# Kernel tuning notes

Measured on AMD Instinct MI355X. Metric: run time of the kernel, lower is better.

## Reference

```python
import jax, jax.numpy as jnp
import numpy as np
from functools import partial


def lstm(x, Wx, Wh, b, act):
    """Keras LSTM. x:[B,T,F]. Gate order i,f,c,o. Returns (all_h:[B,T,H], last_h:[B,H])."""
    B, T, _ = x.shape
    H = Wh.shape[0]
    xz = jnp.einsum('btf,fg->btg', x, Wx) + b  # precompute input projections
    def step(carry, xz_t):
        h, c = carry
        z = xz_t + h @ Wh
        i, f, g, o = jnp.split(z, 4, axis=-1)
        i = jax.nn.sigmoid(i); f = jax.nn.sigmoid(f)
        g = act(g); o = jax.nn.sigmoid(o)
        c = f * c + i * g
        h = o * act(c)
        return (h, c), h
    init = (jnp.zeros((B, H), x.dtype), jnp.zeros((B, H), x.dtype))
    (h_last, _), hs = jax.lax.scan(step, init, jnp.swapaxes(xz, 0, 1))
    return jnp.swapaxes(hs, 0, 1), h_last


def gru(x, Wx, Wh, b):
    """Keras GRU with reset_after=True. b:[2,3H]. Gate order z,r,h. Returns last h."""
    B, T, _ = x.shape
    H = Wh.shape[0]
    xz = jnp.einsum('btf,fg->btg', x, Wx) + b[0]
    def step(h, xz_t):
        rec = h @ Wh + b[1]
        xz_z, xz_r, xz_h = jnp.split(xz_t, 3, axis=-1)
        r_z, r_r, r_h = jnp.split(rec, 3, axis=-1)
        z = jax.nn.sigmoid(xz_z + r_z)
        r = jax.nn.sigmoid(xz_r + r_r)
        hh = jnp.tanh(xz_h + r * r_h)
        h = z * h + (1.0 - z) * hh
        return h, None
    h0 = jnp.zeros((B, H), x.dtype)
    h_last, _ = jax.lax.scan(step, h0, jnp.swapaxes(xz, 0, 1))
    return h_last


def setup_inputs() -> dict:
    key = jax.random.key(0)
    ks = jax.random.split(key, 32)
    s = 0.05  # small init so relu-LSTM stays numerically stable over 64 steps
    d = {}
    d['keypoint_data'] = jax.random.normal(ks[0], (256, 64, 1662), jnp.float32)
    d['img_data'] = jax.random.normal(ks[1], (256, 64, 2048), jnp.float32)
    # keypoint LSTM stack: 1662->64->128->64, gates=4H
    d['kW1x'] = s * jax.random.normal(ks[2], (1662, 256), jnp.float32)
    d['kW1h'] = s * jax.random.normal(ks[3], (64, 256), jnp.float32)
    d['kb1'] = jnp.zeros((256,), jnp.float32)
    d['kW2x'] = s * jax.random.normal(ks[4], (64, 512), jnp.float32)
    d['kW2h'] = s * jax.random.normal(ks[5], (128, 512), jnp.float32)
    d['kb2'] = jnp.zeros((512,), jnp.float32)
    d['kW3x'] = s * jax.random.normal(ks[6], (128, 256), jnp.float32)
    d['kW3h'] = s * jax.random.normal(ks[7], (64, 256), jnp.float32)
    d['kb3'] = jnp.zeros((256,), jnp.float32)
    # keypoint dense heads
    d['kD1w'] = s * jax.random.normal(ks[8], (64, 64), jnp.float32)
    d['kD1b'] = jnp.zeros((64,), jnp.float32)
    d['kD2w'] = s * jax.random.normal(ks[9], (64, 32), jnp.float32)
    d['kD2b'] = jnp.zeros((32,), jnp.float32)
    # img branch: LSTM 2048->64 (tanh), GRU 64->8 (reset_after bias [2,24])
    d['iWx'] = s * jax.random.normal(ks[10], (2048, 256), jnp.float32)
    d['iWh'] = s * jax.random.normal(ks[11], (64, 256), jnp.float32)
    d['ib'] = jnp.zeros((256,), jnp.float32)
    d['gWx'] = s * jax.random.normal(ks[12], (64, 24), jnp.float32)
    d['gWh'] = s * jax.random.normal(ks[13], (8, 24), jnp.float32)
    d['gb'] = jnp.zeros((2, 24), jnp.float32)
    d['iDw'] = s * jax.random.normal(ks[14], (8, 8), jnp.float32)
    d['iDb'] = jnp.zeros((8,), jnp.float32)
    # final dense on concat([img(8), key(32)]) -> num_classes
    d['fW'] = s * jax.random.normal(ks[15], (40, 10), jnp.float32)
    d['fb'] = jnp.zeros((10,), jnp.float32)
    return d


def reference(keypoint_data, img_data,
              kW1x, kW1h, kb1, kW2x, kW2h, kb2, kW3x, kW3h, kb3,
              kD1w, kD1b, kD2w, kD2b,
              iWx, iWh, ib, gWx, gWh, gb, iDw, iDb, fW, fb):
    relu = jax.nn.relu
    # keypoint branch: 3 relu-LSTMs
    h, _ = lstm(keypoint_data, kW1x, kW1h, kb1, relu)
    h, _ = lstm(h, kW2x, kW2h, kb2, relu)
    _, h = lstm(h, kW3x, kW3h, kb3, relu)  # return_sequences=False
    h = relu(h @ kD1w + kD1b)
    key_out = relu(h @ kD2w + kD2b)  # [B,32]
    # img branch: tanh LSTM -> GRU -> (dropout=identity at inference) -> dense
    hs, _ = lstm(img_data, iWx, iWh, ib, jnp.tanh)
    g = gru(hs, gWx, gWh, gb)  # [B,8]
    img_out = relu(g @ iDw + iDb)  # [B,8]
    combined = jnp.concatenate([img_out, key_out], axis=-1)  # [B,40]
    return jax.nn.softmax(combined @ fW + fb, axis=-1)
```

## Files before the change

### kernel.cpp

```cpp
#include <hip/hip_runtime.h>


typedef short bf16x8 __attribute__((ext_vector_type(8)));
typedef float f32x4 __attribute__((ext_vector_type(4)));

__device__ __forceinline__ unsigned f2bf(float x) {
    unsigned u = __float_as_uint(x);
    return (u + 0x7FFFu + ((u >> 16) & 1u)) >> 16;
}
__device__ __forceinline__ float bf2f(unsigned b) { return __uint_as_float(b << 16); }
__device__ __forceinline__ float sigmoidf_(float x) { return 1.f / (1.f + __expf(-x)); }
__device__ __forceinline__ float tanhf_(float x) {
    float e = __expf(2.f * x);
    return 1.f - 2.f / (e + 1.f);
}

template<int K, int N>
__device__ __forceinline__ void split_w(const float* __restrict__ W,
                                        unsigned short* __restrict__ hi,
                                        unsigned short* __restrict__ lo, int item) {
    int kt = item / N;
    int n  = item % N;
    unsigned uh[16], ul[16];
#pragma unroll
    for (int p = 0; p < 16; p++) {
        unsigned h2[2], l2[2];
#pragma unroll
        for (int e = 0; e < 2; e++) {
            int k = kt * 32 + p * 2 + e;
            float x = (k < K) ? W[(size_t)k * N + n] : 0.f;
            unsigned hb = f2bf(x);
            h2[e] = hb;
            l2[e] = f2bf(x - bf2f(hb));
        }
        uh[p] = h2[0] | (h2[1] << 16);
        ul[p] = l2[0] | (l2[1] << 16);
    }
    size_t off = (size_t)(kt * N + n) * 32;
    uint4* dh = (uint4*)(hi + off);
    uint4* dl = (uint4*)(lo + off);
#pragma unroll
    for (int c = 0; c < 4; c++) {
        uint4 v; v.x = uh[c*4]; v.y = uh[c*4+1]; v.z = uh[c*4+2]; v.w = uh[c*4+3];
        dh[c] = v;
        uint4 u; u.x = ul[c*4]; u.y = ul[c*4+1]; u.z = ul[c*4+2]; u.w = ul[c*4+3];
        dl[c] = u;
    }
}

__global__ __launch_bounds__(256) void split_all(
    const float* kW1x, const float* iWx, const float* kW2x, const float* kW3x,
    unsigned short* w1h, unsigned short* w1l, unsigned short* wih, unsigned short* wil,
    unsigned short* w2h, unsigned short* w2l, unsigned short* w3h, unsigned short* w3l) {
    int wid = blockIdx.x * 256 + threadIdx.x;
    if (wid < 13312)       split_w<1662, 256>(kW1x, w1h, w1l, wid);
    else if (wid < 29696)  split_w<2048, 256>(iWx,  wih, wil, wid - 13312);
    else if (wid < 30720)  split_w<64,   512>(kW2x, w2h, w2l, wid - 29696);
    else if (wid < 31744)  split_w<128,  256>(kW3x, w3h, w3l, wid - 30720);
}

__global__ __launch_bounds__(256, 2) void gemm_rd(
    const float* __restrict__ A, const unsigned short* __restrict__ Bhi,
    const unsigned short* __restrict__ Blo, const float* __restrict__ bias,
    float* __restrict__ out0, float* __restrict__ out1,
    int Kreal, int Kt, int Nfull) {
    const int m0  = blockIdx.x * 64;
    const int n0  = blockIdx.y * 256;
    const int ks  = blockIdx.z;
    const int nks = gridDim.z;
    const int ktChunk = (Kt + nks - 1) / nks;
    const int kt0 = ks * ktChunk;
    const int ktEnd = min(Kt, kt0 + ktChunk);
    const int tid = threadIdx.x;
    const int lane = tid & 63;
    const int wv   = tid >> 6;
    const int l15  = lane & 15;
    const int q    = lane >> 4;

    __shared__ unsigned short Ah[2][64 * 40], Al[2][64 * 40];

    f32x4 acc[4][4];
#pragma unroll
    for (int i = 0; i < 4; i++)
#pragma unroll
        for (int j = 0; j < 4; j++) acc[i][j] = (f32x4){0.f, 0.f, 0.f, 0.f};

    auto stage = [&](int kt, int buf) {
#pragma unroll
        for (int it = 0; it < 2; it++) {
            int item = tid + it * 256;
            int row = item >> 3, kg = item & 7;
            int gk = kt * 32 + kg * 4;
            const float* ap = A + (size_t)(m0 + row) * Kreal + gk;
            float x0, x1, x2, x3;
            if (gk + 4 <= Kreal) {
                float2 p0 = *(const float2*)ap;
                float2 p1 = *(const float2*)(ap + 2);
                x0 = p0.x; x1 = p0.y; x2 = p1.x; x3 = p1.y;
            } else {
                x0 = (gk + 0 < Kreal) ? ap[0] : 0.f;
                x1 = (gk + 1 < Kreal) ? ap[1] : 0.f;
                x2 = (gk + 2 < Kreal) ? ap[2] : 0.f;
                x3 = (gk + 3 < Kreal) ? ap[3] : 0.f;
            }
            unsigned h0 = f2bf(x0), h1 = f2bf(x1), h2 = f2bf(x2), h3 = f2bf(x3);
            unsigned l0 = f2bf(x0 - bf2f(h0)), l1 = f2bf(x1 - bf2f(h1));
            unsigned l2 = f2bf(x2 - bf2f(h2)), l3 = f2bf(x3 - bf2f(h3));
            uint2 vh; vh.x = h0 | (h1 << 16); vh.y = h2 | (h3 << 16);
            uint2 vl; vl.x = l0 | (l1 << 16); vl.y = l2 | (l3 << 16);
            *(uint2*)&Ah[buf][row * 40 + kg * 4] = vh;
            *(uint2*)&Al[buf][row * 40 + kg * 4] = vl;
        }
    };

    stage(kt0, 0);
    for (int kt = kt0; kt < ktEnd; kt++) {
        int b = (kt - kt0) & 1;
        bf16x8 bh[4], bl[4];
#pragma unroll
        for (int nt = 0; nt < 4; nt++) {
            size_t boff = ((size_t)kt * Nfull + n0 + wv * 64 + nt * 16 + l15) * 32 + q * 8;
            bh[nt] = *(const bf16x8*)(Bhi + boff);
            bl[nt] = *(const bf16x8*)(Blo + boff);
        }
        __syncthreads();
        if (kt + 1 < ktEnd) stage(kt + 1, b ^ 1);
#pragma unroll
        for (int mt = 0; mt < 4; mt++) {
            int o = (mt * 16 + l15) * 40 + q * 8;
            bf16x8 ah = *(const bf16x8*)&Ah[b][o];
            bf16x8 al = *(const bf16x8*)&Al[b][o];
#pragma unroll
            for (int nt = 0; nt < 4; nt++) {
                acc[mt][nt] = __builtin_amdgcn_mfma_f32_16x16x32_bf16(ah, bh[nt], acc[mt][nt], 0, 0, 0);
                acc[mt][nt] = __builtin_amdgcn_mfma_f32_16x16x32_bf16(ah, bl[nt], acc[mt][nt], 0, 0, 0);
                acc[mt][nt] = __builtin_amdgcn_mfma_f32_16x16x32_bf16(al, bh[nt], acc[mt][nt], 0, 0, 0);
            }
        }
    }
    float* op = (ks == 0) ? out0 : out1;
#pragma unroll
    for (int nt = 0; nt < 4; nt++) {
        int gcol = n0 + wv * 64 + nt * 16 + l15;
        float bv = (ks == 0) ? bias[gcol] : 0.f;
#pragma unroll
        for (int mt = 0; mt < 4; mt++)
#pragma unroll
            for (int r = 0; r < 4; r++) {
                int grow = m0 + mt * 16 + q * 4 + r;
                op[(size_t)grow * Nfull + gcol] = acc[mt][nt][r] + bv;
            }
    }
}

__global__ __launch_bounds__(256) void lstm_h64(
    int nA,
    const float* __restrict__ xA0, const float* __restrict__ xA1,
    const float* __restrict__ WhA, float* __restrict__ hA, int actA,
    const float* __restrict__ xB0, const float* __restrict__ xB1,
    const float* __restrict__ WhB, float* __restrict__ hB, int actB) {
    int bid = blockIdx.x;
    bool sec = bid >= nA;
    int b = sec ? bid - nA : bid;
    const float* x0 = sec ? xB0 : xA0;
    const float* x1 = sec ? xB1 : xA1;
    const float* Wh = sec ? WhB : WhA;
    float* hout     = sec ? hB  : hA;
    int act         = sec ? actB : actA;
    bool has1 = (x1 != nullptr);

    int g = threadIdx.x;
    float w[64];
#pragma unroll
    for (int k = 0; k < 64; k++) w[k] = Wh[k * 256 + g];

    __shared__ alignas(16) float hs[64];
    __shared__ float za[256];
    if (g < 64) hs[g] = 0.f;
    float c = 0.f;
    __syncthreads();

    const float* x0r = x0 + (size_t)b * 64 * 256;
    const float* x1r = has1 ? x1 + (size_t)b * 64 * 256 : x0r;
    float* hr = hout + (size_t)b * 64 * 64;
    bool isc = (g >= 128) && (g < 192);
    float cur = x0r[g] + (has1 ? x1r[g] : 0.f);
    for (int t = 0; t < 64; t++) {
        float nxt = 0.f;
        if (t < 63) {
            nxt = x0r[(t + 1) * 256 + g];
            if (has1) nxt += x1r[(t + 1) * 256 + g];
        }
        float z0 = cur, z1 = 0.f, z2 = 0.f, z3 = 0.f;
#pragma unroll
        for (int kk = 0; kk < 16; kk++) {
            float4 h4 = *(const float4*)&hs[kk * 4];
            float a0 = fmaf(h4.x, w[kk * 4 + 0], fmaf(h4.y, w[kk * 4 + 1], 0.f));
            float a1 = fmaf(h4.z, w[kk * 4 + 2], fmaf(h4.w, w[kk * 4 + 3], 0.f));
            if ((kk & 3) == 0) { z0 += a0; z1 += a1; }
            else if ((kk & 3) == 1) { z2 += a0; z3 += a1; }
            else if ((kk & 3) == 2) { z0 += a0; z1 += a1; }
            else { z2 += a0; z3 += a1; }
        }
        float z = (z0 + z1) + (z2 + z3);
        float a;
        if (isc) a = (act == 0) ? fmaxf(z, 0.f) : tanhf_(z);
        else     a = sigmoidf_(z);
        za[g] = a;
        __syncthreads();
        if (g < 64) {
            float iv = za[g], fv = za[64 + g], cd = za[128 + g], ov = za[192 + g];
            c = fmaf(fv, c, iv * cd);
            float ca = (act == 0) ? fmaxf(c, 0.f) : tanhf_(c);
            float h = ov * ca;
            hs[g] = h;
            hr[t * 64 + g] = h;
        }
        __syncthreads();
        cur = nxt;
    }
}

__global__ __launch_bounds__(512, 2) void lstm_h128(
    const float* __restrict__ xz, const float* __restrict__ Wh, float* __restrict__ hout) {
    int b = blockIdx.x;
    int g = threadIdx.x;
    float w[128];
#pragma unroll
    for (int k = 0; k < 128; k++) w[k] = Wh[k * 512 + g];

    __shared__ alignas(16) float hs[128];
    __shared__ float za[512];
    if (g < 128) hs[g] = 0.f;
    float c = 0.f;
    __syncthreads();

    const float* xzr = xz + (size_t)b * 64 * 512;
    float* hr = hout + (size_t)b * 64 * 128;
    bool isc = (g >= 256) && (g < 384);
    float cur = xzr[g];
    for (int t = 0; t < 64; t++) {
        float nxt = 0.f;
        if (t < 63) nxt = xzr[(t + 1) * 512 + g];
        float z0 = cur, z1 = 0.f, z2 = 0.f, z3 = 0.f;
#pragma unroll
        for (int kk = 0; kk < 32; kk++) {
            float4 h4 = *(const float4*)&hs[kk * 4];
            float a0 = fmaf(h4.x, w[kk * 4 + 0], fmaf(h4.y, w[kk * 4 + 1], 0.f));
            float a1 = fmaf(h4.z, w[kk * 4 + 2], fmaf(h4.w, w[kk * 4 + 3], 0.f));
            if ((kk & 1) == 0) { z0 += a0; z1 += a1; }
            else { z2 += a0; z3 += a1; }
        }
        float z = (z0 + z1) + (z2 + z3);
        float a = isc ? fmaxf(z, 0.f) : sigmoidf_(z);
        za[g] = a;
        __syncthreads();
        if (g < 128) {
            float iv = za[g], fv = za[128 + g], cd = za[256 + g], ov = za[384 + g];
            c = fmaf(fv, c, iv * cd);
            float h = ov * fmaxf(c, 0.f);
            hs[g] = h;
            hr[t * 128 + g] = h;
        }
        __syncthreads();
        cur = nxt;
    }
}

__global__ __launch_bounds__(64) void gru_kernel(
    const float* __restrict__ hsimg, const float* __restrict__ gWx,
    const float* __restrict__ gWh, const float* __restrict__ gb,
    float* __restrict__ glast) {
    int b = blockIdx.x;
    int qq = threadIdx.x;
    int col = (qq < 24) ? qq : 0;
    float wx[64], wh[8];
#pragma unroll
    for (int k = 0; k < 64; k++) wx[k] = gWx[k * 24 + col];
#pragma unroll
    for (int k = 0; k < 8; k++)  wh[k] = gWh[k * 24 + col];
    float b0 = gb[col], b1 = gb[24 + col];

    float hval = 0.f;
    const float* hb = hsimg + (size_t)b * 64 * 64;
    for (int t = 0; t < 64; t++) {
        float s0 = b0, s1 = 0.f, s2 = 0.f, s3 = 0.f;
#pragma unroll
        for (int k = 0; k < 64; k += 4) {
            s0 = fmaf(hb[t * 64 + k + 0], wx[k + 0], s0);
            s1 = fmaf(hb[t * 64 + k + 1], wx[k + 1], s1);
            s2 = fmaf(hb[t * 64 + k + 2], wx[k + 2], s2);
            s3 = fmaf(hb[t * 64 + k + 3], wx[k + 3], s3);
        }
        float sx = (s0 + s1) + (s2 + s3);
        float sr = b1;
#pragma unroll
        for (int k = 0; k < 8; k++) sr = fmaf(__shfl(hval, k), wh[k], sr);
        float xzz = __shfl(sx, qq),      rzz = __shfl(sr, qq);
        float xzr = __shfl(sx, 8 + qq),  rzr = __shfl(sr, 8 + qq);
        float xzh = __shfl(sx, 16 + qq), rzh = __shfl(sr, 16 + qq);
        float zz = sigmoidf_(xzz + rzz);
        float rv = sigmoidf_(xzr + rzr);
        float hc = tanhf_(xzh + rv * rzh);
        hval = zz * hval + (1.f - zz) * hc;
    }
    if (qq < 8) glast[b * 8 + qq] = hval;
}

__global__ __launch_bounds__(64) void final_head(
    const float* __restrict__ h3seq, const float* __restrict__ glast,
    const float* __restrict__ kD1w, const float* __restrict__ kD1b,
    const float* __restrict__ kD2w, const float* __restrict__ kD2b,
    const float* __restrict__ iDw,  const float* __restrict__ iDb,
    const float* __restrict__ fW,   const float* __restrict__ fb,
    float* __restrict__ outp) {
    int b = blockIdx.x * 64 + threadIdx.x;
    float h3[64];
#pragma unroll
    for (int k = 0; k < 64; k++) h3[k] = h3seq[((size_t)b * 64 + 63) * 64 + k];
    float d1[64];
#pragma unroll
    for (int j = 0; j < 64; j++) {
        float s = kD1b[j];
#pragma unroll
        for (int k = 0; k < 64; k++) s = fmaf(h3[k], kD1w[k * 64 + j], s);
        d1[j] = fmaxf(s, 0.f);
    }
    float d2[32];
#pragma unroll
    for (int j = 0; j < 32; j++) {
        float s = kD2b[j];
#pragma unroll
        for (int k = 0; k < 64; k++) s = fmaf(d1[k], kD2w[k * 32 + j], s);
        d2[j] = fmaxf(s, 0.f);
    }
    float gi[8];
#pragma unroll
    for (int k = 0; k < 8; k++) gi[k] = glast[b * 8 + k];
    float io[8];
#pragma unroll
    for (int j = 0; j < 8; j++) {
        float s = iDb[j];
#pragma unroll
        for (int k = 0; k < 8; k++) s = fmaf(gi[k], iDw[k * 8 + j], s);
        io[j] = fmaxf(s, 0.f);
    }
    float lg[10];
#pragma unroll
    for (int j = 0; j < 10; j++) {
        float s = fb[j];
#pragma unroll
        for (int k = 0; k < 8; k++)  s = fmaf(io[k], fW[k * 10 + j], s);
#pragma unroll
        for (int k = 0; k < 32; k++) s = fmaf(d2[k], fW[(8 + k) * 10 + j], s);
        lg[j] = s;
    }
    float mx = lg[0];
#pragma unroll
    for (int j = 1; j < 10; j++) mx = fmaxf(mx, lg[j]);
    float den = 0.f, ex[10];
#pragma unroll
    for (int j = 0; j < 10; j++) { ex[j] = __expf(lg[j] - mx); den += ex[j]; }
    float inv = 1.f / den;
#pragma unroll
    for (int j = 0; j < 10; j++) outp[b * 10 + j] = ex[j] * inv;
}

extern "C" void kernel_launch(void* const* d_in, const int* in_sizes, int n_in,
                              void* d_out, int out_size, void* d_ws, size_t ws_size,
                              hipStream_t stream) {
    const float* keypoint = (const float*)d_in[0];
    const float* img      = (const float*)d_in[1];
    const float* kW1x = (const float*)d_in[2];
    const float* kW1h = (const float*)d_in[3];
    const float* kb1  = (const float*)d_in[4];
    const float* kW2x = (const float*)d_in[5];
    const float* kW2h = (const float*)d_in[6];
    const float* kb2  = (const float*)d_in[7];
    const float* kW3x = (const float*)d_in[8];
    const float* kW3h = (const float*)d_in[9];
    const float* kb3  = (const float*)d_in[10];
    const float* kD1w = (const float*)d_in[11];
    const float* kD1b = (const float*)d_in[12];
    const float* kD2w = (const float*)d_in[13];
    const float* kD2b = (const float*)d_in[14];
    const float* iWx  = (const float*)d_in[15];
    const float* iWh  = (const float*)d_in[16];
    const float* ib   = (const float*)d_in[17];
    const float* gWx  = (const float*)d_in[18];
    const float* gWh  = (const float*)d_in[19];
    const float* gb   = (const float*)d_in[20];
    const float* iDw  = (const float*)d_in[21];
    const float* iDb  = (const float*)d_in[22];
    const float* fW   = (const float*)d_in[23];
    const float* fb   = (const float*)d_in[24];
    float* outp = (float*)d_out;

    char* ws = (char*)d_ws;
    const size_t MB16 = (size_t)16384 * 256 * 4;
    float* r1a = (float*)(ws);
    float* r1b = (float*)(ws + MB16);
    float* r2a = (float*)(ws + 2 * MB16);
    float* r2b = (float*)(ws + 3 * MB16);
    size_t off = 4 * MB16;
    float* h1seq = (float*)(ws + off); off += (size_t)16384 * 64 * 4;
    float* h2seq = (float*)(ws + off); off += (size_t)16384 * 128 * 4;
    float* hsimg = (float*)(ws + off); off += (size_t)16384 * 64 * 4;
    float* glast = (float*)(ws + off); off += (size_t)256 * 8 * 4;
    unsigned short* w1h = (unsigned short*)(ws + off); off += (size_t)52 * 256 * 32 * 2;
    unsigned short* w1l = (unsigned short*)(ws + off); off += (size_t)52 * 256 * 32 * 2;
    unsigned short* wih = (unsigned short*)(ws + off); off += (size_t)64 * 256 * 32 * 2;
    unsigned short* wil = (unsigned short*)(ws + off); off += (size_t)64 * 256 * 32 * 2;
    unsigned short* w2h = (unsigned short*)(ws + off); off += (size_t)2 * 512 * 32 * 2;
    unsigned short* w2l = (unsigned short*)(ws + off); off += (size_t)2 * 512 * 32 * 2;
    unsigned short* w3h = (unsigned short*)(ws + off); off += (size_t)4 * 256 * 32 * 2;
    unsigned short* w3l = (unsigned short*)(ws + off); off += (size_t)4 * 256 * 32 * 2;
    float* xz2   = r2a;
    float* h3seq = h1seq;

    split_all<<<124, 256, 0, stream>>>(kW1x, iWx, kW2x, kW3x,
                                       w1h, w1l, wih, wil, w2h, w2l, w3h, w3l);
    gemm_rd<<<dim3(256, 1, 2), 256, 0, stream>>>(keypoint, w1h, w1l, kb1, r1a, r1b, 1662, 52, 256);
    gemm_rd<<<dim3(256, 1, 2), 256, 0, stream>>>(img, wih, wil, ib, r2a, r2b, 2048, 64, 256);
    lstm_h64<<<512, 256, 0, stream>>>(256, r1a, r1b, kW1h, h1seq, 0, r2a, r2b, iWh, hsimg, 1);
    gemm_rd<<<dim3(256, 2, 1), 256, 0, stream>>>(h1seq, w2h, w2l, kb2, xz2, xz2, 64, 2, 512);
    lstm_h128<<<256, 512, 0, stream>>>(xz2, kW2h, h2seq);
    gemm_rd<<<dim3(256, 1, 2), 256, 0, stream>>>(h2seq, w3h, w3l, kb3, r1a, r1b, 128, 4, 256);
    lstm_h64<<<256, 256, 0, stream>>>(256, r1a, r1b, kW3h, h3seq, 0, r1a, r1b, kW3h, h3seq, 0);
    gru_kernel<<<256, 64, 0, stream>>>(hsimg, gWx, gWh, gb, glast);
    final_head<<<4, 64, 0, stream>>>(h3seq, glast, kD1w, kD1b, kD2w, kD2b,
                                     iDw, iDb, fW, fb, outp);
    (void)in_sizes; (void)n_in; (void)out_size; (void)ws_size;
}
```

Before: 754.6 us.

## Restructure GEMM A staging into register-prefetched double k-tiles; simplify recurrent dot loops

```diff
diff --git a/kernel.cpp b/kernel.cpp
--- a/kernel.cpp
+++ b/kernel.cpp
@@ -68,16 +68,18 @@
     const int n0  = blockIdx.y * 256;
     const int ks  = blockIdx.z;
     const int nks = gridDim.z;
-    const int ktChunk = (Kt + nks - 1) / nks;
+    const int ktChunk = Kt / nks;
     const int kt0 = ks * ktChunk;
-    const int ktEnd = min(Kt, kt0 + ktChunk);
+    const int G   = ktChunk / 2;
     const int tid = threadIdx.x;
     const int lane = tid & 63;
     const int wv   = tid >> 6;
     const int l15  = lane & 15;
     const int q    = lane >> 4;
-
-    __shared__ unsigned short Ah[2][64 * 40], Al[2][64 * 40];
+    const int row  = tid >> 2;
+    const int kc   = tid & 3;
+
+    __shared__ unsigned short Ah[2][2][64 * 40], Al[2][2][64 * 40];
 
     f32x4 acc[4][4];
 #pragma unroll
@@ -85,58 +87,76 @@
 #pragma unroll
         for (int j = 0; j < 4; j++) acc[i][j] = (f32x4){0.f, 0.f, 0.f, 0.f};
 
-    auto stage = [&](int kt, int buf) {
-#pragma unroll
-        for (int it = 0; it < 2; it++) {
-            int item = tid + it * 256;
-            int row = item >> 3, kg = item & 7;
-            int gk = kt * 32 + kg * 4;
-            const float* ap = A + (size_t)(m0 + row) * Kreal + gk;
-            float x0, x1, x2, x3;
-            if (gk + 4 <= Kreal) {
-                float2 p0 = *(const float2*)ap;
-                float2 p1 = *(const float2*)(ap + 2);
-                x0 = p0.x; x1 = p0.y; x2 = p1.x; x3 = p1.y;
+    auto loadA = [&](int g, float* r) {
+        int kb = (kt0 + 2 * g) * 32 + kc * 16;
+        const float* ap = A + (size_t)(m0 + row) * Kreal + kb;
+#pragma unroll
+        for (int j = 0; j < 8; j++) {
+            int gk = kb + 2 * j;
+            if (gk + 2 <= Kreal) {
+                float2 p = *(const float2*)(ap + 2 * j);
+                r[2*j] = p.x; r[2*j+1] = p.y;
             } else {
-                x0 = (gk + 0 < Kreal) ? ap[0] : 0.f;
-                x1 = (gk + 1 < Kreal) ? ap[1] : 0.f;
-                x2 = (gk + 2 < Kreal) ? ap[2] : 0.f;
-                x3 = (gk + 3 < Kreal) ? ap[3] : 0.f;
+                r[2*j]   = (gk < Kreal) ? ap[2*j] : 0.f;
+                r[2*j+1] = 0.f;
             }
-            unsigned h0 = f2bf(x0), h1 = f2bf(x1), h2 = f2bf(x2), h3 = f2bf(x3);
-            unsigned l0 = f2bf(x0 - bf2f(h0)), l1 = f2bf(x1 - bf2f(h1));
-            unsigned l2 = f2bf(x2 - bf2f(h2)), l3 = f2bf(x3 - bf2f(h3));
-            uint2 vh; vh.x = h0 | (h1 << 16); vh.y = h2 | (h3 << 16);
-            uint2 vl; vl.x = l0 | (l1 << 16); vl.y = l2 | (l3 << 16);
-            *(uint2*)&Ah[buf][row * 40 + kg * 4] = vh;
-            *(uint2*)&Al[buf][row * 40 + kg * 4] = vl;
         }
     };
-
-    stage(kt0, 0);
-    for (int kt = kt0; kt < ktEnd; kt++) {
-        int b = (kt - kt0) & 1;
-        bf16x8 bh[4], bl[4];
-#pragma unroll
-        for (int nt = 0; nt < 4; nt++) {
-            size_t boff = ((size_t)kt * Nfull + n0 + wv * 64 + nt * 16 + l15) * 32 + q * 8;
-            bh[nt] = *(const bf16x8*)(Bhi + boff);
-            bl[nt] = *(const bf16x8*)(Blo + boff);
-        }
+    auto writeA = [&](int buf, const float* r) {
+        int sub = kc >> 1;
+        int kk0 = (kc & 1) * 16;
+        unsigned ph[8], pl[8];
+#pragma unroll
+        for (int p = 0; p < 8; p++) {
+            unsigned h0 = f2bf(r[2*p]),   h1 = f2bf(r[2*p+1]);
+            unsigned l0 = f2bf(r[2*p] - bf2f(h0));
+            unsigned l1 = f2bf(r[2*p+1] - bf2f(h1));
+            ph[p] = h0 | (h1 << 16);
+            pl[p] = l0 | (l1 << 16);
+        }
+        uint4* dh = (uint4*)&Ah[buf][sub][row * 40 + kk0];
+        uint4* dl = (uint4*)&Al[buf][sub][row * 40 + kk0];
+        uint4 v0; v0.x = ph[0]; v0.y = ph[1]; v0.z = ph[2]; v0.w = ph[3];
+        uint4 v1; v1.x = ph[4]; v1.y = ph[5]; v1.z = ph[6]; v1.w = ph[7];
+        dh[0] = v0; dh[1] = v1;
+        uint4 u0; u0.x = pl[0]; u0.y = pl[1]; u0.z = pl[2]; u0.w = pl[3];
+        uint4 u1; u1.x = pl[4]; u1.y = pl[5]; u1.z = pl[6]; u1.w = pl[7];
+        dl[0] = u0; dl[1] = u1;
+    };
+
+    float r0[16];
+    loadA(0, r0);
+    writeA(0, r0);
+
+    for (int g = 0; g < G; g++) {
+        int buf = g & 1;
         __syncthreads();
-        if (kt + 1 < ktEnd) stage(kt + 1, b ^ 1);
-#pragma unroll
-        for (int mt = 0; mt < 4; mt++) {
-            int o = (mt * 16 + l15) * 40 + q * 8;
-            bf16x8 ah = *(const bf16x8*)&Ah[b][o];
-            bf16x8 al = *(const bf16x8*)&Al[b][o];
+        float rn[16];
+        if (g + 1 < G) loadA(g + 1, rn);
+#pragma unroll
+        for (int sub = 0; sub < 2; sub++) {
+            int ktg = kt0 + 2 * g + sub;
+            bf16x8 bh[4], bl[4];
 #pragma unroll
             for (int nt = 0; nt < 4; nt++) {
-                acc[mt][nt] = __builtin_amdgcn_mfma_f32_16x16x32_bf16(ah, bh[nt], acc[mt][nt], 0, 0, 0);
-                acc[mt][nt] = __builtin_amdgcn_mfma_f32_16x16x32_bf16(ah, bl[nt], acc[mt][nt], 0, 0, 0);
-                acc[mt][nt] = __builtin_amdgcn_mfma_f32_16x16x32_bf16(al, bh[nt], acc[mt][nt], 0, 0, 0);
+                size_t boff = ((size_t)ktg * Nfull + n0 + wv * 64 + nt * 16 + l15) * 32 + q * 8;
+                bh[nt] = *(const bf16x8*)(Bhi + boff);
+                bl[nt] = *(const bf16x8*)(Blo + boff);
             }
-        }
+#pragma unroll
+            for (int mt = 0; mt < 4; mt++) {
+                int o = (mt * 16 + l15) * 40 + q * 8;
+                bf16x8 ah = *(const bf16x8*)&Ah[buf][sub][o];
+                bf16x8 al = *(const bf16x8*)&Al[buf][sub][o];
+#pragma unroll
+                for (int nt = 0; nt < 4; nt++) {
+                    acc[mt][nt] = __builtin_amdgcn_mfma_f32_16x16x32_bf16(ah, bh[nt], acc[mt][nt], 0, 0, 0);
+                    acc[mt][nt] = __builtin_amdgcn_mfma_f32_16x16x32_bf16(ah, bl[nt], acc[mt][nt], 0, 0, 0);
+                    acc[mt][nt] = __builtin_amdgcn_mfma_f32_16x16x32_bf16(al, bh[nt], acc[mt][nt], 0, 0, 0);
+                }
+            }
+        }
+        if (g + 1 < G) writeA(buf ^ 1, rn);
     }
     float* op = (ks == 0) ? out0 : out1;
 #pragma unroll
@@ -195,12 +215,10 @@
 #pragma unroll
         for (int kk = 0; kk < 16; kk++) {
             float4 h4 = *(const float4*)&hs[kk * 4];
-            float a0 = fmaf(h4.x, w[kk * 4 + 0], fmaf(h4.y, w[kk * 4 + 1], 0.f));
-            float a1 = fmaf(h4.z, w[kk * 4 + 2], fmaf(h4.w, w[kk * 4 + 3], 0.f));
-            if ((kk & 3) == 0) { z0 += a0; z1 += a1; }
-            else if ((kk & 3) == 1) { z2 += a0; z3 += a1; }
-            else if ((kk & 3) == 2) { z0 += a0; z1 += a1; }
-            else { z2 += a0; z3 += a1; }
+            z0 = fmaf(h4.x, w[kk * 4 + 0], z0);
+            z1 = fmaf(h4.y, w[kk * 4 + 1], z1);
+            z2 = fmaf(h4.z, w[kk * 4 + 2], z2);
+            z3 = fmaf(h4.w, w[kk * 4 + 3], z3);
         }
         float z = (z0 + z1) + (z2 + z3);
         float a;
@@ -246,10 +264,10 @@
 #pragma unroll
         for (int kk = 0; kk < 32; kk++) {
             float4 h4 = *(const float4*)&hs[kk * 4];
-            float a0 = fmaf(h4.x, w[kk * 4 + 0], fmaf(h4.y, w[kk * 4 + 1], 0.f));
-            float a1 = fmaf(h4.z, w[kk * 4 + 2], fmaf(h4.w, w[kk * 4 + 3], 0.f));
-            if ((kk & 1) == 0) { z0 += a0; z1 += a1; }
-            else { z2 += a0; z3 += a1; }
+            z0 = fmaf(h4.x, w[kk * 4 + 0], z0);
+            z1 = fmaf(h4.y, w[kk * 4 + 1], z1);
+            z2 = fmaf(h4.z, w[kk * 4 + 2], z2);
+            z3 = fmaf(h4.w, w[kk * 4 + 3], z3);
         }
         float z = (z0 + z1) + (z2 + z3);
         float a = isc ? fmaxf(z, 0.f) : sigmoidf_(z);
@@ -283,14 +301,16 @@
 
     float hval = 0.f;
     const float* hb = hsimg + (size_t)b * 64 * 64;
+    float cur = hb[qq];
     for (int t = 0; t < 64; t++) {
+        float nxt = (t < 63) ? hb[(t + 1) * 64 + qq] : 0.f;
         float s0 = b0, s1 = 0.f, s2 = 0.f, s3 = 0.f;
 #pragma unroll
         for (int k = 0; k < 64; k += 4) {
-            s0 = fmaf(hb[t * 64 + k + 0], wx[k + 0], s0);
-            s1 = fmaf(hb[t * 64 + k + 1], wx[k + 1], s1);
-            s2 = fmaf(hb[t * 64 + k + 2], wx[k + 2], s2);
-            s3 = fmaf(hb[t * 64 + k + 3], wx[k + 3], s3);
+            s0 = fmaf(__shfl(cur, k + 0), wx[k + 0], s0);
+            s1 = fmaf(__shfl(cur, k + 1), wx[k + 1], s1);
+            s2 = fmaf(__shfl(cur, k + 2), wx[k + 2], s2);
+            s3 = fmaf(__shfl(cur, k + 3), wx[k + 3], s3);
         }
         float sx = (s0 + s1) + (s2 + s3);
         float sr = b1;
@@ -303,6 +323,7 @@
         float rv = sigmoidf_(xzr + rzr);
         float hc = tanhf_(xzh + rv * rzh);
         hval = zz * hval + (1.f - zz) * hc;
+        cur = nxt;
     }
     if (qq < 8) glast[b * 8 + qq] = hval;
 }
```

Result: faster. 700.3 us (-7.2%).
